# Performance work log

Hardware: AMD Instinct MI355X
Metric: run time of the kernel (lower is better)

## Reference

```python
import jax, jax.numpy as jnp
import numpy as np

EMBED_DIM = 512
NUM_HEADS = 8
HEAD_DIM = EMBED_DIM // NUM_HEADS


def setup_inputs() -> dict:
    key = jax.random.key(0)
    ks = jax.random.split(key, 9)
    s = 1.0 / np.sqrt(EMBED_DIM)
    x = jax.random.normal(ks[0], (2, 4096, EMBED_DIM), dtype=jnp.float32)
    return {
        "x": x,
        "Wq": jax.random.uniform(ks[1], (EMBED_DIM, EMBED_DIM), jnp.float32, -s, s),
        "bq": jax.random.uniform(ks[2], (EMBED_DIM,), jnp.float32, -s, s),
        "Wk": jax.random.uniform(ks[3], (EMBED_DIM, EMBED_DIM), jnp.float32, -s, s),
        "bk": jax.random.uniform(ks[4], (EMBED_DIM,), jnp.float32, -s, s),
        "Wv": jax.random.uniform(ks[5], (EMBED_DIM, EMBED_DIM), jnp.float32, -s, s),
        "bv": jax.random.uniform(ks[6], (EMBED_DIM,), jnp.float32, -s, s),
        "Wo": jax.random.uniform(ks[7], (EMBED_DIM, EMBED_DIM), jnp.float32, -s, s),
        "bo": jax.random.uniform(ks[8], (EMBED_DIM,), jnp.float32, -s, s),
    }


def reference(x, Wq, bq, Wk, bk, Wv, bv, Wo, bo):
    B, S, E = x.shape
    H, D = NUM_HEADS, HEAD_DIM
    # projections (torch Linear: x @ W.T + b)
    q = (x @ Wq.T + bq).reshape(B, S, H, D).transpose(0, 2, 1, 3)  # [B,H,S,D]
    k = (x @ Wk.T + bk).reshape(B, S, H, D).transpose(0, 2, 1, 3)
    v = (x @ Wv.T + bv).reshape(B, S, H, D).transpose(0, 2, 1, 3)
    scores = jnp.einsum("bhsd,bhtd->bhst", q, k) / np.sqrt(D)  # [B,H,S,S]
    attn = jax.nn.softmax(scores, axis=-1)
    out = jnp.einsum("bhst,bhtd->bhsd", attn, v)  # [B,H,S,D]
    out = out.transpose(0, 2, 1, 3).reshape(B, S, E)
    return out @ Wo.T + bo + x
```

## Files before the change

kernel.cpp:

```cpp
#include <hip/hip_runtime.h>
#include <hip/hip_bf16.h>


typedef __attribute__((ext_vector_type(8))) short short8;
typedef __attribute__((ext_vector_type(4))) short short4v;
typedef __attribute__((ext_vector_type(4))) float floatx4;
typedef __attribute__((ext_vector_type(2))) float floatx2;

#define SEQ 4096
#define EMB 512
#define NH 8
#define HD 64
#define MROWS 8192
#define SC2 0.18033688011112042f

__device__ inline unsigned short f2bf_rne(float f) {
    union { float f; unsigned int u; } c; c.f = f;
    unsigned int u = c.u;
    return (unsigned short)((u + 0x7FFFu + ((u >> 16) & 1u)) >> 16);
}

__device__ inline short8 load8f(const float* __restrict__ p) {
    float4 a = *(const float4*)p;
    float4 b = *(const float4*)(p + 4);
    short8 r;
    r[0] = (short)f2bf_rne(a.x); r[1] = (short)f2bf_rne(a.y);
    r[2] = (short)f2bf_rne(a.z); r[3] = (short)f2bf_rne(a.w);
    r[4] = (short)f2bf_rne(b.x); r[5] = (short)f2bf_rne(b.y);
    r[6] = (short)f2bf_rne(b.z); r[7] = (short)f2bf_rne(b.w);
    return r;
}

__device__ inline void gload_lds16(const unsigned short* g, unsigned short* l) {
    __builtin_amdgcn_global_load_lds(
        (__attribute__((address_space(1))) void*)(void*)g,
        (__attribute__((address_space(3))) void*)l,
        16, 0, 0);
}

__device__ inline unsigned int pk_bf2(float a, float b) {
    union { float f; unsigned int u; } ca, cb; ca.f = a; cb.f = b;
    return __builtin_amdgcn_perm(cb.u + 0x8000u, ca.u + 0x8000u, 0x07060302u);
}

__device__ inline unsigned int pk_bf2t(float a, float b) {
    union { float f; unsigned int u; } ca, cb; ca.f = a; cb.f = b;
    return __builtin_amdgcn_perm(cb.u, ca.u, 0x07060302u);
}

__global__ __launch_bounds__(256) void convert_kernel(
    const float* __restrict__ x, const float* __restrict__ Wq,
    const float* __restrict__ Wk, const float* __restrict__ Wv,
    const float* __restrict__ Wo, unsigned short* __restrict__ xb,
    unsigned short* __restrict__ wb)
{
    const size_t i8 = ((size_t)blockIdx.x * 256 + threadIdx.x) * 8;
    const float* src; unsigned short* dst;
    if (i8 < (size_t)MROWS * EMB) { src = x + i8; dst = xb + i8; }
    else {
        size_t j = i8 - (size_t)MROWS * EMB;
        int w = (int)(j >> 18); size_t off = j & 262143;
        src = (w == 0 ? Wq : w == 1 ? Wk : w == 2 ? Wv : Wo) + off;
        dst = wb + (size_t)w * 262144 + off;
    }
    *(short8*)dst = load8f(src);
}

__global__ __launch_bounds__(256) void qkv_kernel(
    const unsigned short* __restrict__ xb, const unsigned short* __restrict__ wb,
    const float* __restrict__ bq, const float* __restrict__ bk,
    const float* __restrict__ bv, unsigned short* __restrict__ Qo,
    unsigned short* __restrict__ Ko, unsigned short* __restrict__ VTo)
{
    __shared__ unsigned short smem[32768];

    const int tid = threadIdx.x, wave = tid >> 6, lane = tid & 63;
    const int quad = lane >> 4, l16 = lane & 15;
    const int wm = wave >> 1, wn = wave & 1;
    const int row0 = blockIdx.x * 128, col0 = blockIdx.y * 128;
    const int z = blockIdx.z;

    unsigned short* sA = smem;
    unsigned short* sB = smem + 16384;

    const unsigned short* A = xb + (size_t)row0 * EMB;
    const unsigned short* Bm = wb + (size_t)z * 262144 + (size_t)col0 * EMB;
    const float* bias = z == 0 ? bq : z == 1 ? bk : bv;
    unsigned short* out = z == 0 ? Qo : z == 1 ? Ko : VTo;

    auto stage = [&](int buf, int k0) {
#pragma unroll
        for (int it = 0; it < 4; ++it) {
            const int s = it * 256 + tid;
            const int row = s >> 3, cg = (s & 7) ^ (row & 7);
            const size_t go = (size_t)row * EMB + k0 + cg * 8;
            gload_lds16(A + go, &sA[buf * 8192 + (it * 256 + wave * 64) * 8]);
            gload_lds16(Bm + go, &sB[buf * 8192 + (it * 256 + wave * 64) * 8]);
        }
    };

    floatx4 acc[4][4];
#pragma unroll
    for (int i = 0; i < 4; ++i)
#pragma unroll
        for (int j = 0; j < 4; ++j) { floatx4 zz = {0.f,0.f,0.f,0.f}; acc[i][j] = zz; }

    stage(0, 0);
    int buf = 0;
    for (int k0 = 0; k0 < EMB; k0 += 64) {
        __syncthreads();
        if (k0 + 64 < EMB) stage(buf ^ 1, k0 + 64);
#pragma unroll
        for (int kk = 0; kk < 2; ++kk) {
            short8 a[4], b[4];
#pragma unroll
            for (int mi = 0; mi < 4; ++mi)
                a[mi] = *(const short8*)&sA[buf * 8192 + (wm * 64 + mi * 16 + l16) * 64 + (((kk * 4 + quad) ^ (l16 & 7)) << 3)];
#pragma unroll
            for (int ni = 0; ni < 4; ++ni)
                b[ni] = *(const short8*)&sB[buf * 8192 + (wn * 64 + ni * 16 + l16) * 64 + (((kk * 4 + quad) ^ (l16 & 7)) << 3)];
            if (z != 2) {
#pragma unroll
                for (int i = 0; i < 4; ++i)
#pragma unroll
                    for (int j = 0; j < 4; ++j)
                        acc[i][j] = __builtin_amdgcn_mfma_f32_16x16x32_bf16(b[i], a[j], acc[i][j], 0, 0, 0);
            } else {
#pragma unroll
                for (int i = 0; i < 4; ++i)
#pragma unroll
                    for (int j = 0; j < 4; ++j)
                        acc[i][j] = __builtin_amdgcn_mfma_f32_16x16x32_bf16(a[i], b[j], acc[i][j], 0, 0, 0);
            }
        }
        buf ^= 1;
    }

    __syncthreads();
    unsigned short* ct = smem;
    const float qs = (z == 0) ? SC2 : 1.0f;
    if (z != 2) {
#pragma unroll
        for (int i = 0; i < 4; ++i) {
            const int n0 = wn * 64 + i * 16 + quad * 4;
            const float4 fb = *(const float4*)&bias[col0 + n0];
#pragma unroll
            for (int j = 0; j < 4; ++j) {
                const int m = wm * 64 + j * 16 + l16;
                ushort4 pk;
                pk.x = f2bf_rne((acc[i][j][0] + fb.x) * qs);
                pk.y = f2bf_rne((acc[i][j][1] + fb.y) * qs);
                pk.z = f2bf_rne((acc[i][j][2] + fb.z) * qs);
                pk.w = f2bf_rne((acc[i][j][3] + fb.w) * qs);
                *(ushort4*)&ct[m * 132 + n0] = pk;
            }
        }
    } else {
#pragma unroll
        for (int j = 0; j < 4; ++j) {
            const int n = wn * 64 + j * 16 + l16;
            const float fb = bias[col0 + n];
#pragma unroll
            for (int i = 0; i < 4; ++i) {
                const int m0 = wm * 64 + i * 16 + quad * 4;
                ushort4 pk;
                pk.x = f2bf_rne(acc[i][j][0] + fb);
                pk.y = f2bf_rne(acc[i][j][1] + fb);
                pk.z = f2bf_rne(acc[i][j][2] + fb);
                pk.w = f2bf_rne(acc[i][j][3] + fb);
                *(ushort4*)&ct[n * 132 + m0] = pk;
            }
        }
    }
    __syncthreads();
#pragma unroll
    for (int it = 0; it < 8; ++it) {
        const int idx = it * 256 + tid;
        const int row = idx >> 4, chunk = idx & 15;
        short8 v = *(const short8*)&ct[row * 132 + chunk * 8];
        size_t addr;
        if (z != 2) {
            const int m_g = row0 + row;
            const int b = m_g >> 12, s = m_g & 4095;
            const int n_g = col0 + chunk * 8;
            const int h = n_g >> 6, d = n_g & 63;
            addr = ((size_t)((b * NH + h) * SEQ + s)) * HD + d;
        } else {
            const int n_g = col0 + row;
            const int h = n_g >> 6, d = n_g & 63;
            const int m_g = row0 + chunk * 8;
            const int b = m_g >> 12, s0 = m_g & 4095;
            addr = ((size_t)((b * NH + h) * HD + d)) * SEQ + s0;
        }
        *(short8*)&out[addr] = v;
    }
}

__global__ __launch_bounds__(256) void attn_kernel(
    const unsigned short* __restrict__ Q, const unsigned short* __restrict__ K,
    const unsigned short* __restrict__ VT, unsigned short* __restrict__ Oout)
{
    __shared__ unsigned short sK[2][2][4096];
    __shared__ unsigned short sVT[2][2][4096];

    const int tid = threadIdx.x, wave = tid >> 6, lane = tid & 63;
    const int quad = lane >> 4, l16 = lane & 15;
    const int bh = blockIdx.x, q0 = blockIdx.y * 128;
    const int xm = l16 & 7;

    const unsigned short* Qh = Q + (size_t)bh * SEQ * HD;
    const unsigned short* Kh = K + (size_t)bh * SEQ * HD;
    const unsigned short* Vh = VT + (size_t)bh * HD * SEQ;

    short8 qf[2][2];
#pragma unroll
    for (int mi = 0; mi < 2; ++mi)
#pragma unroll
        for (int kk = 0; kk < 2; ++kk)
            qf[mi][kk] = *(const short8*)(Qh + (size_t)(q0 + wave * 32 + mi * 16 + l16) * HD + kk * 32 + quad * 8);

    floatx4 oacc[2][4];
#pragma unroll
    for (int mi = 0; mi < 2; ++mi)
#pragma unroll
        for (int dt = 0; dt < 4; ++dt) { floatx4 zz = {0.f,0.f,0.f,0.f}; oacc[mi][dt] = zz; }
    floatx2 psum2[2] = {{0.f, 0.f}, {0.f, 0.f}};
    const floatx4 z4 = {0.f, 0.f, 0.f, 0.f};

    auto stage = [&](int buf, int t0) {
#pragma unroll
        for (int sub = 0; sub < 2; ++sub)
#pragma unroll
            for (int psi = 0; psi < 2; ++psi) {
                const int r = psi * 32 + wave * 8 + (lane >> 3);
                const int c = (lane & 7) ^ (r & 7);
                gload_lds16(Kh + (size_t)(t0 + sub * 64 + r) * HD + c * 8,
                            &sK[buf][sub][psi * 2048 + wave * 512]);
                gload_lds16(Vh + (size_t)r * SEQ + t0 + sub * 64 + c * 8,
                            &sVT[buf][sub][psi * 2048 + wave * 512]);
            }
    };

    stage(0, 0);
    int buf = 0;
    for (int t0 = 0; t0 < SEQ; t0 += 128) {
        __syncthreads();
        if (t0 + 128 < SEQ) stage(buf ^ 1, t0 + 128);

#pragma unroll
        for (int sub = 0; sub < 2; ++sub) {
            const unsigned short* sKs  = sK[buf][sub];
            const unsigned short* sVTs = sVT[buf][sub];

            floatx4 stf[2][4];
            {
                short8 bK[4];
#pragma unroll
                for (int nt = 0; nt < 4; ++nt)
                    bK[nt] = *(const short8*)&sKs[(nt * 16 + l16) * 64 + ((quad ^ xm) << 3)];
#pragma unroll
                for (int mi = 0; mi < 2; ++mi)
#pragma unroll
                    for (int nt = 0; nt < 4; ++nt)
                        stf[mi][nt] = __builtin_amdgcn_mfma_f32_16x16x32_bf16(bK[nt], qf[mi][0], z4, 0, 0, 0);
            }
            {
                short8 bK[4];
#pragma unroll
                for (int nt = 0; nt < 4; ++nt)
                    bK[nt] = *(const short8*)&sKs[(nt * 16 + l16) * 64 + (((4 + quad) ^ xm) << 3)];
#pragma unroll
                for (int mi = 0; mi < 2; ++mi)
#pragma unroll
                    for (int nt = 0; nt < 4; ++nt)
                        stf[mi][nt] = __builtin_amdgcn_mfma_f32_16x16x32_bf16(bK[nt], qf[mi][1], stf[mi][nt], 0, 0, 0);
            }

            short4v paf[2][4];
#pragma unroll
            for (int mi = 0; mi < 2; ++mi)
#pragma unroll
                for (int nt = 0; nt < 4; ++nt) {
                    const float p0 = __builtin_amdgcn_exp2f(stf[mi][nt][0]);
                    const float p1 = __builtin_amdgcn_exp2f(stf[mi][nt][1]);
                    const float p2 = __builtin_amdgcn_exp2f(stf[mi][nt][2]);
                    const float p3 = __builtin_amdgcn_exp2f(stf[mi][nt][3]);
                    floatx2 a = {p0, p1}, b = {p2, p3};
                    psum2[mi] += a + b;
                    union { uint2 u; short4v s; } cv;
                    cv.u.x = pk_bf2t(p0, p1);
                    cv.u.y = pk_bf2t(p2, p3);
                    paf[mi][nt] = cv.s;
                }

#pragma unroll
            for (int nt = 0; nt < 4; ++nt) {
                short4v bv[4];
#pragma unroll
                for (int dt = 0; dt < 4; ++dt)
                    bv[dt] = *(const short4v*)&sVTs[(dt * 16 + l16) * 64 +
                             (((nt * 2 + (quad >> 1)) ^ xm) << 3) + (quad & 1) * 4];
#pragma unroll
                for (int mi = 0; mi < 2; ++mi)
#pragma unroll
                    for (int dt = 0; dt < 4; ++dt)
                        oacc[mi][dt] = __builtin_amdgcn_mfma_f32_16x16x16bf16_1k(paf[mi][nt], bv[dt], oacc[mi][dt], 0, 0, 0);
            }
        }
        buf ^= 1;
    }

    float psum[2];
#pragma unroll
    for (int mi = 0; mi < 2; ++mi) {
        psum[mi] = psum2[mi][0] + psum2[mi][1];
        psum[mi] += __shfl_xor(psum[mi], 16);
        psum[mi] += __shfl_xor(psum[mi], 32);
    }

    const int b = bh >> 3, h = bh & 7;
#pragma unroll
    for (int mi = 0; mi < 2; ++mi)
#pragma unroll
        for (int r = 0; r < 4; ++r) {
            const float inv = 1.0f / __shfl(psum[mi], quad * 4 + r);
            const int s = q0 + wave * 32 + mi * 16 + quad * 4 + r;
            const size_t base = ((size_t)b * SEQ + s) * EMB + h * HD;
#pragma unroll
            for (int dt = 0; dt < 4; ++dt)
                Oout[base + dt * 16 + l16] = f2bf_rne(oacc[mi][dt][r] * inv);
        }
}

__global__ __launch_bounds__(256) void outproj_kernel(
    const unsigned short* __restrict__ Ain, const unsigned short* __restrict__ wob,
    const float* __restrict__ bias, const float* __restrict__ X,
    float* __restrict__ out)
{
    __shared__ unsigned short sA[2][4096];
    __shared__ unsigned short sB[2][8192];

    const int tid = threadIdx.x, wave = tid >> 6, lane = tid & 63;
    const int quad = lane >> 4, l16 = lane & 15;
    const int wm = wave >> 1, wn = wave & 1;
    const int row0 = blockIdx.x * 64, col0 = blockIdx.y * 128;

    const unsigned short* A = Ain + (size_t)row0 * EMB;
    const unsigned short* Bm = wob + (size_t)col0 * EMB;

    auto stage = [&](int buf, int k0) {
#pragma unroll
        for (int it = 0; it < 2; ++it) {
            const int s = it * 256 + tid;
            const int row = s >> 3, cg = (s & 7) ^ (row & 7);
            gload_lds16(A + (size_t)row * EMB + k0 + cg * 8, &sA[buf][(it * 256 + wave * 64) * 8]);
        }
#pragma unroll
        for (int it = 0; it < 4; ++it) {
            const int s = it * 256 + tid;
            const int row = s >> 3, cg = (s & 7) ^ (row & 7);
            gload_lds16(Bm + (size_t)row * EMB + k0 + cg * 8, &sB[buf][(it * 256 + wave * 64) * 8]);
        }
    };

    floatx4 acc[2][4];
#pragma unroll
    for (int mi = 0; mi < 2; ++mi)
#pragma unroll
        for (int ni = 0; ni < 4; ++ni) { floatx4 zz = {0.f,0.f,0.f,0.f}; acc[mi][ni] = zz; }

    stage(0, 0);
    int buf = 0;
    for (int k0 = 0; k0 < EMB; k0 += 64) {
        __syncthreads();
        if (k0 + 64 < EMB) stage(buf ^ 1, k0 + 64);
#pragma unroll
        for (int kk = 0; kk < 2; ++kk) {
            short8 a[2], b[4];
#pragma unroll
            for (int mi = 0; mi < 2; ++mi)
                a[mi] = *(const short8*)&sA[buf][(wm * 32 + mi * 16 + l16) * 64 + (((kk * 4 + quad) ^ (l16 & 7)) << 3)];
#pragma unroll
            for (int ni = 0; ni < 4; ++ni)
                b[ni] = *(const short8*)&sB[buf][(wn * 64 + ni * 16 + l16) * 64 + (((kk * 4 + quad) ^ (l16 & 7)) << 3)];
#pragma unroll
            for (int mi = 0; mi < 2; ++mi)
#pragma unroll
                for (int ni = 0; ni < 4; ++ni)
                    acc[mi][ni] = __builtin_amdgcn_mfma_f32_16x16x32_bf16(a[mi], b[ni], acc[mi][ni], 0, 0, 0);
        }
        buf ^= 1;
    }

#pragma unroll
    for (int mi = 0; mi < 2; ++mi)
#pragma unroll
        for (int ni = 0; ni < 4; ++ni) {
            const int n = col0 + wn * 64 + ni * 16 + l16;
            const float bs = bias[n];
#pragma unroll
            for (int r = 0; r < 4; ++r) {
                const int m = row0 + wm * 32 + mi * 16 + quad * 4 + r;
                const size_t idx = (size_t)m * EMB + n;
                out[idx] = acc[mi][ni][r] + bs + X[idx];
            }
        }
}

extern "C" void kernel_launch(void* const* d_in, const int* in_sizes, int n_in,
                              void* d_out, int out_size, void* d_ws, size_t ws_size,
                              hipStream_t stream) {
    const float* x  = (const float*)d_in[0];
    const float* Wq = (const float*)d_in[1];
    const float* bq = (const float*)d_in[2];
    const float* Wk = (const float*)d_in[3];
    const float* bk = (const float*)d_in[4];
    const float* Wv = (const float*)d_in[5];
    const float* bv = (const float*)d_in[6];
    const float* Wo = (const float*)d_in[7];
    const float* bo = (const float*)d_in[8];
    float* out = (float*)d_out;

    const size_t SZ = (size_t)MROWS * EMB;
    unsigned short* wsXB = (unsigned short*)d_ws;
    unsigned short* wsWB = wsXB + SZ;
    unsigned short* wsQ  = wsWB + 4 * 262144;
    unsigned short* wsK  = wsQ + SZ;
    unsigned short* wsVT = wsK + SZ;

    convert_kernel<<<2560, 256, 0, stream>>>(x, Wq, Wk, Wv, Wo, wsXB, wsWB);
    qkv_kernel<<<dim3(MROWS / 128, EMB / 128, 3), 256, 0, stream>>>(
        wsXB, wsWB, bq, bk, bv, wsQ, wsK, wsVT);
    attn_kernel<<<dim3(2 * NH, SEQ / 128), 256, 0, stream>>>(wsQ, wsK, wsVT, wsXB);
    outproj_kernel<<<dim3(MROWS / 64, EMB / 128), 256, 0, stream>>>(
        wsXB, wsWB + 3 * 262144, bo, x, out);
}
```

Baseline: 199.3 us.

## Use 8 waves of 16 query rows and 16x16x32 MFMA for PV in attention

```diff
diff --git a/kernel.cpp b/kernel.cpp
--- a/kernel.cpp
+++ b/kernel.cpp
@@ -196,7 +196,7 @@
     }
 }
 
-__global__ __launch_bounds__(256) void attn_kernel(
+__global__ __launch_bounds__(512) void attn_kernel(
     const unsigned short* __restrict__ Q, const unsigned short* __restrict__ K,
     const unsigned short* __restrict__ VT, unsigned short* __restrict__ Oout)
 {
@@ -212,33 +212,37 @@
     const unsigned short* Kh = K + (size_t)bh * SEQ * HD;
     const unsigned short* Vh = VT + (size_t)bh * HD * SEQ;
 
-    short8 qf[2][2];
-#pragma unroll
-    for (int mi = 0; mi < 2; ++mi)
-#pragma unroll
-        for (int kk = 0; kk < 2; ++kk)
-            qf[mi][kk] = *(const short8*)(Qh + (size_t)(q0 + wave * 32 + mi * 16 + l16) * HD + kk * 32 + quad * 8);
-
-    floatx4 oacc[2][4];
-#pragma unroll
-    for (int mi = 0; mi < 2; ++mi)
-#pragma unroll
-        for (int dt = 0; dt < 4; ++dt) { floatx4 zz = {0.f,0.f,0.f,0.f}; oacc[mi][dt] = zz; }
-    floatx2 psum2[2] = {{0.f, 0.f}, {0.f, 0.f}};
+    short8 qf[2];
+#pragma unroll
+    for (int kk = 0; kk < 2; ++kk)
+        qf[kk] = *(const short8*)(Qh + (size_t)(q0 + wave * 16 + l16) * HD + kk * 32 + quad * 8);
+
+    int kbase[4], kx0[4], kx1[4];
+#pragma unroll
+    for (int nt = 0; nt < 4; ++nt) {
+        const int g = nt >> 1, T = nt & 1;
+        const int R = g * 32 + ((l16 >> 2) << 3) + (T << 2) + (l16 & 3);
+        const int fR = (R & 7) ^ ((R >> 2) & 7);
+        kbase[nt] = R * 64;
+        kx0[nt] = (quad ^ fR) << 3;
+        kx1[nt] = ((4 + quad) ^ fR) << 3;
+    }
+
+    floatx4 oacc[4];
+#pragma unroll
+    for (int dt = 0; dt < 4; ++dt) { floatx4 zz = {0.f,0.f,0.f,0.f}; oacc[dt] = zz; }
+    floatx2 psum2 = {0.f, 0.f};
     const floatx4 z4 = {0.f, 0.f, 0.f, 0.f};
 
     auto stage = [&](int buf, int t0) {
-#pragma unroll
-        for (int sub = 0; sub < 2; ++sub)
-#pragma unroll
-            for (int psi = 0; psi < 2; ++psi) {
-                const int r = psi * 32 + wave * 8 + (lane >> 3);
-                const int c = (lane & 7) ^ (r & 7);
-                gload_lds16(Kh + (size_t)(t0 + sub * 64 + r) * HD + c * 8,
-                            &sK[buf][sub][psi * 2048 + wave * 512]);
-                gload_lds16(Vh + (size_t)r * SEQ + t0 + sub * 64 + c * 8,
-                            &sVT[buf][sub][psi * 2048 + wave * 512]);
-            }
+        const int r = tid >> 3, j = tid & 7;
+        const int cK = j ^ ((r & 7) ^ ((r >> 2) & 7));
+        const int cV = j ^ (r & 7);
+#pragma unroll
+        for (int sub = 0; sub < 2; ++sub) {
+            gload_lds16(Kh + (size_t)(t0 + sub * 64 + r) * HD + cK * 8, &sK[buf][sub][wave * 512]);
+            gload_lds16(Vh + (size_t)r * SEQ + t0 + sub * 64 + cV * 8, &sVT[buf][sub][wave * 512]);
+        }
     };
 
     stage(0, 0);
@@ -252,84 +256,74 @@
             const unsigned short* sKs  = sK[buf][sub];
             const unsigned short* sVTs = sVT[buf][sub];
 
-            floatx4 stf[2][4];
+            floatx4 stf[4];
             {
                 short8 bK[4];
 #pragma unroll
                 for (int nt = 0; nt < 4; ++nt)
-                    bK[nt] = *(const short8*)&sKs[(nt * 16 + l16) * 64 + ((quad ^ xm) << 3)];
-#pragma unroll
-                for (int mi = 0; mi < 2; ++mi)
-#pragma unroll
-                    for (int nt = 0; nt < 4; ++nt)
-                        stf[mi][nt] = __builtin_amdgcn_mfma_f32_16x16x32_bf16(bK[nt], qf[mi][0], z4, 0, 0, 0);
+                    bK[nt] = *(const short8*)&sKs[kbase[nt] + kx0[nt]];
+#pragma unroll
+                for (int nt = 0; nt < 4; ++nt)
+                    stf[nt] = __builtin_amdgcn_mfma_f32_16x16x32_bf16(bK[nt], qf[0], z4, 0, 0, 0);
             }
             {
                 short8 bK[4];
 #pragma unroll
                 for (int nt = 0; nt < 4; ++nt)
-                    bK[nt] = *(const short8*)&sKs[(nt * 16 + l16) * 64 + (((4 + quad) ^ xm) << 3)];
-#pragma unroll
-                for (int mi = 0; mi < 2; ++mi)
-#pragma unroll
-                    for (int nt = 0; nt < 4; ++nt)
-                        stf[mi][nt] = __builtin_amdgcn_mfma_f32_16x16x32_bf16(bK[nt], qf[mi][1], stf[mi][nt], 0, 0, 0);
-            }
-
-            short4v paf[2][4];
-#pragma unroll
-            for (int mi = 0; mi < 2; ++mi)
-#pragma unroll
-                for (int nt = 0; nt < 4; ++nt) {
-                    const float p0 = __builtin_amdgcn_exp2f(stf[mi][nt][0]);
-                    const float p1 = __builtin_amdgcn_exp2f(stf[mi][nt][1]);
-                    const float p2 = __builtin_amdgcn_exp2f(stf[mi][nt][2]);
-                    const float p3 = __builtin_amdgcn_exp2f(stf[mi][nt][3]);
-                    floatx2 a = {p0, p1}, b = {p2, p3};
-                    psum2[mi] += a + b;
-                    union { uint2 u; short4v s; } cv;
-                    cv.u.x = pk_bf2t(p0, p1);
-                    cv.u.y = pk_bf2t(p2, p3);
-                    paf[mi][nt] = cv.s;
-                }
-
-#pragma unroll
-            for (int nt = 0; nt < 4; ++nt) {
-                short4v bv[4];
+                    bK[nt] = *(const short8*)&sKs[kbase[nt] + kx1[nt]];
+#pragma unroll
+                for (int nt = 0; nt < 4; ++nt)
+                    stf[nt] = __builtin_amdgcn_mfma_f32_16x16x32_bf16(bK[nt], qf[1], stf[nt], 0, 0, 0);
+            }
+
+            short8 paf[2];
+#pragma unroll
+            for (int g = 0; g < 2; ++g) {
+                float e[8];
+#pragma unroll
+                for (int T = 0; T < 2; ++T)
+#pragma unroll
+                    for (int r = 0; r < 4; ++r)
+                        e[T * 4 + r] = __builtin_amdgcn_exp2f(stf[g * 2 + T][r]);
+                floatx2 pa = {e[0], e[1]}, pb = {e[2], e[3]};
+                floatx2 pc = {e[4], e[5]}, pd = {e[6], e[7]};
+                psum2 += (pa + pb) + (pc + pd);
+                union { uint4 u; short8 s; } cv;
+                cv.u.x = pk_bf2t(e[0], e[1]);
+                cv.u.y = pk_bf2t(e[2], e[3]);
+                cv.u.z = pk_bf2t(e[4], e[5]);
+                cv.u.w = pk_bf2t(e[6], e[7]);
+                paf[g] = cv.s;
+            }
+
+#pragma unroll
+            for (int g = 0; g < 2; ++g) {
+                short8 bv8[4];
 #pragma unroll
                 for (int dt = 0; dt < 4; ++dt)
-                    bv[dt] = *(const short4v*)&sVTs[(dt * 16 + l16) * 64 +
-                             (((nt * 2 + (quad >> 1)) ^ xm) << 3) + (quad & 1) * 4];
-#pragma unroll
-                for (int mi = 0; mi < 2; ++mi)
-#pragma unroll
-                    for (int dt = 0; dt < 4; ++dt)
-                        oacc[mi][dt] = __builtin_amdgcn_mfma_f32_16x16x16bf16_1k(paf[mi][nt], bv[dt], oacc[mi][dt], 0, 0, 0);
+                    bv8[dt] = *(const short8*)&sVTs[(dt * 16 + l16) * 64 + (((g * 4 + quad) ^ xm) << 3)];
+#pragma unroll
+                for (int dt = 0; dt < 4; ++dt)
+                    oacc[dt] = __builtin_amdgcn_mfma_f32_16x16x32_bf16(paf[g], bv8[dt], oacc[dt], 0, 0, 0);
             }
         }
         buf ^= 1;
     }
 
-    float psum[2];
-#pragma unroll
-    for (int mi = 0; mi < 2; ++mi) {
-        psum[mi] = psum2[mi][0] + psum2[mi][1];
-        psum[mi] += __shfl_xor(psum[mi], 16);
-        psum[mi] += __shfl_xor(psum[mi], 32);
-    }
+    float psum = psum2[0] + psum2[1];
+    psum += __shfl_xor(psum, 16);
+    psum += __shfl_xor(psum, 32);
 
     const int b = bh >> 3, h = bh & 7;
 #pragma unroll
-    for (int mi = 0; mi < 2; ++mi)
-#pragma unroll
-        for (int r = 0; r < 4; ++r) {
-            const float inv = 1.0f / __shfl(psum[mi], quad * 4 + r);
-            const int s = q0 + wave * 32 + mi * 16 + quad * 4 + r;
-            const size_t base = ((size_t)b * SEQ + s) * EMB + h * HD;
-#pragma unroll
-            for (int dt = 0; dt < 4; ++dt)
-                Oout[base + dt * 16 + l16] = f2bf_rne(oacc[mi][dt][r] * inv);
-        }
+    for (int r = 0; r < 4; ++r) {
+        const float inv = 1.0f / __shfl(psum, quad * 4 + r);
+        const int s = q0 + wave * 16 + quad * 4 + r;
+        const size_t base = ((size_t)b * SEQ + s) * EMB + h * HD;
+#pragma unroll
+        for (int dt = 0; dt < 4; ++dt)
+            Oout[base + dt * 16 + l16] = f2bf_rne(oacc[dt][r] * inv);
+    }
 }
 
 __global__ __launch_bounds__(256) void outproj_kernel(
@@ -431,7 +425,7 @@
     convert_kernel<<<2560, 256, 0, stream>>>(x, Wq, Wk, Wv, Wo, wsXB, wsWB);
     qkv_kernel<<<dim3(MROWS / 128, EMB / 128, 3), 256, 0, stream>>>(
         wsXB, wsWB, bq, bk, bv, wsQ, wsK, wsVT);
-    attn_kernel<<<dim3(2 * NH, SEQ / 128), 256, 0, stream>>>(wsQ, wsK, wsVT, wsXB);
+    attn_kernel<<<dim3(2 * NH, SEQ / 128), 512, 0, stream>>>(wsQ, wsK, wsVT, wsXB);
     outproj_kernel<<<dim3(MROWS / 64, EMB / 128), 256, 0, stream>>>(
         wsXB, wsWB + 3 * 262144, bo, x, out);
 }
```

After: 192.4 us. -3.5%, faster.

## Use 16x16x32 MFMA for PV by permuting K rows to match P layout

Applied to the files above, without the earlier changes.

```diff
diff --git a/kernel.cpp b/kernel.cpp
--- a/kernel.cpp
+++ b/kernel.cpp
@@ -219,6 +219,17 @@
         for (int kk = 0; kk < 2; ++kk)
             qf[mi][kk] = *(const short8*)(Qh + (size_t)(q0 + wave * 32 + mi * 16 + l16) * HD + kk * 32 + quad * 8);
 
+    int kbase[4], kx0[4], kx1[4];
+#pragma unroll
+    for (int nt = 0; nt < 4; ++nt) {
+        const int g = nt >> 1, T = nt & 1;
+        const int R = g * 32 + ((l16 >> 2) << 3) + (T << 2) + (l16 & 3);
+        const int fR = (R & 7) ^ ((R >> 2) & 7);
+        kbase[nt] = R * 64;
+        kx0[nt] = (quad ^ fR) << 3;
+        kx1[nt] = ((4 + quad) ^ fR) << 3;
+    }
+
     floatx4 oacc[2][4];
 #pragma unroll
     for (int mi = 0; mi < 2; ++mi)
@@ -233,10 +244,12 @@
 #pragma unroll
             for (int psi = 0; psi < 2; ++psi) {
                 const int r = psi * 32 + wave * 8 + (lane >> 3);
-                const int c = (lane & 7) ^ (r & 7);
-                gload_lds16(Kh + (size_t)(t0 + sub * 64 + r) * HD + c * 8,
+                const int j = lane & 7;
+                const int cK = j ^ ((r & 7) ^ ((r >> 2) & 7));
+                const int cV = j ^ (r & 7);
+                gload_lds16(Kh + (size_t)(t0 + sub * 64 + r) * HD + cK * 8,
                             &sK[buf][sub][psi * 2048 + wave * 512]);
-                gload_lds16(Vh + (size_t)r * SEQ + t0 + sub * 64 + c * 8,
+                gload_lds16(Vh + (size_t)r * SEQ + t0 + sub * 64 + cV * 8,
                             &sVT[buf][sub][psi * 2048 + wave * 512]);
             }
     };
@@ -257,7 +270,7 @@
                 short8 bK[4];
 #pragma unroll
                 for (int nt = 0; nt < 4; ++nt)
-                    bK[nt] = *(const short8*)&sKs[(nt * 16 + l16) * 64 + ((quad ^ xm) << 3)];
+                    bK[nt] = *(const short8*)&sKs[kbase[nt] + kx0[nt]];
 #pragma unroll
                 for (int mi = 0; mi < 2; ++mi)
 #pragma unroll
@@ -268,7 +281,7 @@
                 short8 bK[4];
 #pragma unroll
                 for (int nt = 0; nt < 4; ++nt)
-                    bK[nt] = *(const short8*)&sKs[(nt * 16 + l16) * 64 + (((4 + quad) ^ xm) << 3)];
+                    bK[nt] = *(const short8*)&sKs[kbase[nt] + kx1[nt]];
 #pragma unroll
                 for (int mi = 0; mi < 2; ++mi)
 #pragma unroll
@@ -276,36 +289,42 @@
                         stf[mi][nt] = __builtin_amdgcn_mfma_f32_16x16x32_bf16(bK[nt], qf[mi][1], stf[mi][nt], 0, 0, 0);
             }
 
-            short4v paf[2][4];
+            short8 bvAll[2][4];
+#pragma unroll
+            for (int g = 0; g < 2; ++g)
+#pragma unroll
+                for (int dt = 0; dt < 4; ++dt)
+                    bvAll[g][dt] = *(const short8*)&sVTs[(dt * 16 + l16) * 64 + (((g * 4 + quad) ^ xm) << 3)];
+
+            short8 paf[2][2];
 #pragma unroll
             for (int mi = 0; mi < 2; ++mi)
 #pragma unroll
-                for (int nt = 0; nt < 4; ++nt) {
-                    const float p0 = __builtin_amdgcn_exp2f(stf[mi][nt][0]);
-                    const float p1 = __builtin_amdgcn_exp2f(stf[mi][nt][1]);
-                    const float p2 = __builtin_amdgcn_exp2f(stf[mi][nt][2]);
-                    const float p3 = __builtin_amdgcn_exp2f(stf[mi][nt][3]);
-                    floatx2 a = {p0, p1}, b = {p2, p3};
-                    psum2[mi] += a + b;
-                    union { uint2 u; short4v s; } cv;
-                    cv.u.x = pk_bf2t(p0, p1);
-                    cv.u.y = pk_bf2t(p2, p3);
-                    paf[mi][nt] = cv.s;
+                for (int g = 0; g < 2; ++g) {
+                    float e[8];
+#pragma unroll
+                    for (int T = 0; T < 2; ++T)
+#pragma unroll
+                        for (int r = 0; r < 4; ++r)
+                            e[T * 4 + r] = __builtin_amdgcn_exp2f(stf[mi][g * 2 + T][r]);
+                    floatx2 pa = {e[0], e[1]}, pb = {e[2], e[3]};
+                    floatx2 pc = {e[4], e[5]}, pd = {e[6], e[7]};
+                    psum2[mi] += (pa + pb) + (pc + pd);
+                    union { uint4 u; short8 s; } cv;
+                    cv.u.x = pk_bf2t(e[0], e[1]);
+                    cv.u.y = pk_bf2t(e[2], e[3]);
+                    cv.u.z = pk_bf2t(e[4], e[5]);
+                    cv.u.w = pk_bf2t(e[6], e[7]);
+                    paf[mi][g] = cv.s;
                 }
 
 #pragma unroll
-            for (int nt = 0; nt < 4; ++nt) {
-                short4v bv[4];
-#pragma unroll
-                for (int dt = 0; dt < 4; ++dt)
-                    bv[dt] = *(const short4v*)&sVTs[(dt * 16 + l16) * 64 +
-                             (((nt * 2 + (quad >> 1)) ^ xm) << 3) + (quad & 1) * 4];
+            for (int g = 0; g < 2; ++g)
 #pragma unroll
                 for (int mi = 0; mi < 2; ++mi)
 #pragma unroll
                     for (int dt = 0; dt < 4; ++dt)
-                        oacc[mi][dt] = __builtin_amdgcn_mfma_f32_16x16x16bf16_1k(paf[mi][nt], bv[dt], oacc[mi][dt], 0, 0, 0);
-            }
+                        oacc[mi][dt] = __builtin_amdgcn_mfma_f32_16x16x32_bf16(paf[mi][g], bvAll[g][dt], oacc[mi][dt], 0, 0, 0);
         }
         buf ^= 1;
     }
```

After: 193.9 us. -2.7%, faster.
